# Optimization experiments

Hardware: AMD Instinct MI355X
Metric: run time of the kernel (lower is better)

## Reference

```python
import jax, jax.numpy as jnp
import numpy as np

N, E, F, H, O, G = 50000, 800000, 50, 512, 121, 20
EPS = 1e-5


def _lin(k, out_f, in_f):
    return jax.random.normal(k, (out_f, in_f), jnp.float32) / np.sqrt(in_f)


def setup_inputs() -> dict:
    key = jax.random.key(0)
    ks = jax.random.split(key, 32)
    inp = {
        "x": jax.random.normal(ks[0], (N, F), jnp.float32),
        "edge_index": jax.random.randint(ks[1], (2, E), 0, N, jnp.int64 if jax.config.jax_enable_x64 else jnp.int32),
        "batch": jnp.sort(jax.random.randint(ks[2], (N,), 0, G, jnp.int32)),
    }
    dims = [(F, H), (H, H), (H, H), (H, H), (H, O)]
    ki = 3
    for i, (fi, fo) in enumerate(dims, start=1):
        inp[f"W{i}l"] = _lin(ks[ki], fo, fi); ki += 1
        inp[f"W{i}r"] = _lin(ks[ki], fo, fi); ki += 1
        inp[f"b{i}"] = jnp.zeros((fo,), jnp.float32)
    for i in range(1, 5):
        inp[f"g{i}"] = jnp.ones((H,), jnp.float32)    # GraphNorm weight
        inp[f"bn{i}"] = jnp.zeros((H,), jnp.float32)  # GraphNorm bias
        inp[f"a{i}"] = jnp.ones((H,), jnp.float32)    # GraphNorm mean_scale
    return inp


def _sage(x, src, dst, inv_deg, Wl, Wr, b):
    # mean aggregation of neighbor messages x[src] at dst, then two linears
    agg = jax.ops.segment_sum(x[src], dst, num_segments=N) * inv_deg  # [N, Fin]
    return agg @ Wl.T + x @ Wr.T + b


def _gnorm(x, batch, inv_sz, w, b, alpha):
    mean = jax.ops.segment_sum(x, batch, num_segments=G) * inv_sz  # [G, C]
    out = x - alpha * mean[batch]
    var = jax.ops.segment_sum(out * out, batch, num_segments=G) * inv_sz
    return out * jax.lax.rsqrt(var[batch] + EPS) * w + b


def reference(x, edge_index, batch,
              W1l, W1r, b1, W2l, W2r, b2, W3l, W3r, b3, W4l, W4r, b4, W5l, W5r, b5,
              g1, bn1, a1, g2, bn2, a2, g3, bn3, a3, g4, bn4, a4):
    src, dst = edge_index[0], edge_index[1]
    deg = jax.ops.segment_sum(jnp.ones((E,), jnp.float32), dst, num_segments=N)
    inv_deg = (1.0 / jnp.maximum(deg, 1.0))[:, None]
    sz = jax.ops.segment_sum(jnp.ones((N,), jnp.float32), batch, num_segments=G)
    inv_sz = (1.0 / jnp.maximum(sz, 1.0))[:, None]

    h = _sage(x, src, dst, inv_deg, W1l, W1r, b1)
    h = jax.nn.relu(_gnorm(h, batch, inv_sz, g1, bn1, a1))  # dropout=identity (eval)
    h = _sage(h, src, dst, inv_deg, W2l, W2r, b2)
    h = jax.nn.relu(_gnorm(h, batch, inv_sz, g2, bn2, a2))
    h = _sage(h, src, dst, inv_deg, W3l, W3r, b3)
    h = jax.nn.relu(_gnorm(h, batch, inv_sz, g3, bn3, a3))
    h = _sage(h, src, dst, inv_deg, W4l, W4r, b4)
    h = jax.nn.relu(_gnorm(h, batch, inv_sz, g4, bn4, a4))
    return _sage(h, src, dst, inv_deg, W5l, W5r, b5)
```

## Files before the change

### kernel.cpp

```cpp
#include <hip/hip_runtime.h>
#include <cstddef>
#include <cstdint>

#define N_NODES 50000
#define N_EDGES 800000
#define F_IN 50
#define K1PAD 64
#define H_DIM 512
#define O_DIM 121
#define N_GROUPS 20
#define EPSV 1e-5f
#define M_PAD 50048
#define M_TILES 391

#define STAT_SPLITS 32
#define SCAN_BLK 256
#define SCAN_NBLK ((N_NODES + SCAN_BLK - 1) / SCAN_BLK)
#define WALL_EL 1769472

typedef unsigned short u16;
typedef __attribute__((ext_vector_type(8))) short short8;
typedef __attribute__((ext_vector_type(8))) unsigned short u16x8;
typedef __attribute__((ext_vector_type(4))) float f32x4;

__device__ __forceinline__ float b2f(u16 u) {
  union { unsigned int i; float f; } v; v.i = ((unsigned int)u) << 16; return v.f;
}
__device__ __forceinline__ u16 f2b(float f) {
  union { float f; unsigned int i; } v; v.f = f;
  unsigned int x = v.i;
  return (u16)((x + 0x7fffu + ((x >> 16) & 1u)) >> 16);
}

__device__ __forceinline__ void gl_lds16(const void* g, void* l) {
  __builtin_amdgcn_global_load_lds(
      (__attribute__((address_space(1))) void*)(g),
      (__attribute__((address_space(3))) void*)(l), 16, 0, 0);
}


__global__ void k_deg(const int* __restrict__ dst, int* __restrict__ deg) {
  int e = blockIdx.x * blockDim.x + threadIdx.x;
  if (e < N_EDGES) atomicAdd(&deg[dst[e]], 1);
}

__global__ void k_scan1(const int* __restrict__ deg, int* __restrict__ off,
                        int* __restrict__ bsum) {
  __shared__ int buf[SCAN_BLK];
  int gid = blockIdx.x * SCAN_BLK + threadIdx.x;
  buf[threadIdx.x] = (gid < N_NODES) ? deg[gid] : 0;
  __syncthreads();
  for (int d = 1; d < SCAN_BLK; d <<= 1) {
    int t = (threadIdx.x >= d) ? buf[threadIdx.x - d] : 0;
    __syncthreads();
    buf[threadIdx.x] += t;
    __syncthreads();
  }
  if (gid < N_NODES) off[gid + 1] = buf[threadIdx.x];
  if (threadIdx.x == SCAN_BLK - 1) bsum[blockIdx.x] = buf[threadIdx.x];
}

__global__ void k_scan2(int* __restrict__ bsum) {
  __shared__ int buf[256];
  int t = threadIdx.x;
  buf[t] = (t < SCAN_NBLK) ? bsum[t] : 0;
  __syncthreads();
  for (int d = 1; d < 256; d <<= 1) {
    int v = (t >= d) ? buf[t - d] : 0;
    __syncthreads();
    buf[t] += v;
    __syncthreads();
  }
  if (t < SCAN_NBLK) bsum[t] = buf[t];
}

__global__ void k_scan3prep(int* __restrict__ off, const int* __restrict__ bsum,
                            const int* __restrict__ deg, float* __restrict__ inv_deg,
                            int* __restrict__ cursor) {
  int gid = blockIdx.x * SCAN_BLK + threadIdx.x;
  if (gid < N_NODES) {
    int add = (blockIdx.x > 0) ? bsum[blockIdx.x - 1] : 0;
    int v = off[gid + 1] + add;
    off[gid + 1] = v;
    if (gid + 1 < N_NODES) cursor[gid + 1] = v;
    inv_deg[gid] = 1.0f / (float)max(deg[gid], 1);
  }
  if (gid == 0) { off[0] = 0; cursor[0] = 0; }
}

__global__ void k_scatter(const int* __restrict__ src, const int* __restrict__ dst,
                          int* __restrict__ cursor, int* __restrict__ csr_src) {
  int e = blockIdx.x * blockDim.x + threadIdx.x;
  if (e < N_EDGES) {
    int p = atomicAdd(&cursor[dst[e]], 1);
    csr_src[p] = src[e];
  }
}

__global__ void k_gbounds(const int* __restrict__ batch, int* __restrict__ gstart,
                          float* __restrict__ inv_sz) {
  int g = threadIdx.x;
  if (g <= N_GROUPS) {
    int lo = 0, hi = N_NODES;
    while (lo < hi) {
      int mid = (lo + hi) >> 1;
      if (batch[mid] < g) lo = mid + 1; else hi = mid;
    }
    gstart[g] = lo;
  }
  __syncthreads();
  if (g < N_GROUPS) {
    int sz = gstart[g + 1] - gstart[g];
    inv_sz[g] = 1.0f / (float)max(sz, 1);
  }
}


__global__ void k_xpad(const float* __restrict__ x, u16* __restrict__ xb) {
  int i = blockIdx.x * blockDim.x + threadIdx.x;
  if (i >= M_PAD * K1PAD) return;
  int r = i >> 6, c = i & (K1PAD - 1);
  float v = (r < N_NODES && c < F_IN) ? x[r * F_IN + c] : 0.f;
  xb[i] = f2b(v);
}

struct WcSrc { const float* p[10]; };
__global__ void k_wconv_all(WcSrc s, u16* __restrict__ wall) {
  int idx = blockIdx.x * blockDim.x + threadIdx.x;
  if (idx >= WALL_EL) return;
  const int seg_start[10] = {0, 32768, 65536, 327680, 589824, 851968,
                             1114112, 1376256, 1638400, 1703936};
  const int jr[10]  = {512, 512, 512, 512, 512, 512, 512, 512, 121, 121};
  const int kin[10] = {50, 50, 512, 512, 512, 512, 512, 512, 512, 512};
  const int ksh[10] = {6, 6, 9, 9, 9, 9, 9, 9, 9, 9};
  int sgi = 0;
#pragma unroll
  for (int t = 1; t < 10; ++t)
    if (idx >= seg_start[t]) sgi = t;
  int local = idx - seg_start[sgi];
  int j = local >> ksh[sgi];
  int k = local & ((1 << ksh[sgi]) - 1);
  float v = (j < jr[sgi] && k < kin[sgi]) ? s.p[sgi][j * kin[sgi] + k] : 0.f;
  wall[idx] = f2b(v);
}


__global__ void k_agg_small(const u16* __restrict__ xb, const int* __restrict__ off,
                            const int* __restrict__ srcs, const float* __restrict__ inv_deg,
                            u16* __restrict__ agg) {
  int n = blockIdx.x;
  int f = threadIdx.x;
  int b = off[n], e = off[n + 1];
  float s = 0.f;
  for (int i = b; i < e; ++i) s += b2f(xb[(size_t)srcs[i] * K1PAD + f]);
  agg[(size_t)n * K1PAD + f] = f2b(s * inv_deg[n]);
}

__global__ __launch_bounds__(256) void k_agg512(
    const u16* __restrict__ h, const int* __restrict__ off,
    const int* __restrict__ srcs, const float* __restrict__ inv_deg,
    u16* __restrict__ agg) {
  int n = blockIdx.x * 4 + threadIdx.y;
  if (n >= N_NODES) return;
  int t = threadIdx.x;
  int b = off[n], e = off[n + 1];
  float a[8] = {0.f, 0.f, 0.f, 0.f, 0.f, 0.f, 0.f, 0.f};
  int i = b;
  for (; i + 8 <= e; i += 8) {
    u16x8 v0 = ((const u16x8*)(h + (size_t)srcs[i + 0] * H_DIM))[t];
    u16x8 v1 = ((const u16x8*)(h + (size_t)srcs[i + 1] * H_DIM))[t];
    u16x8 v2 = ((const u16x8*)(h + (size_t)srcs[i + 2] * H_DIM))[t];
    u16x8 v3 = ((const u16x8*)(h + (size_t)srcs[i + 3] * H_DIM))[t];
    u16x8 v4 = ((const u16x8*)(h + (size_t)srcs[i + 4] * H_DIM))[t];
    u16x8 v5 = ((const u16x8*)(h + (size_t)srcs[i + 5] * H_DIM))[t];
    u16x8 v6 = ((const u16x8*)(h + (size_t)srcs[i + 6] * H_DIM))[t];
    u16x8 v7 = ((const u16x8*)(h + (size_t)srcs[i + 7] * H_DIM))[t];
#pragma unroll
    for (int j = 0; j < 8; ++j)
      a[j] += ((b2f(v0[j]) + b2f(v1[j])) + (b2f(v2[j]) + b2f(v3[j]))) +
              ((b2f(v4[j]) + b2f(v5[j])) + (b2f(v6[j]) + b2f(v7[j])));
  }
  for (; i < e; ++i) {
    u16x8 v0 = ((const u16x8*)(h + (size_t)srcs[i] * H_DIM))[t];
#pragma unroll
    for (int j = 0; j < 8; ++j) a[j] += b2f(v0[j]);
  }
  float w = inv_deg[n];
  u16x8 r;
#pragma unroll
  for (int j = 0; j < 8; ++j) r[j] = f2b(a[j] * w);
  ((u16x8*)(agg + (size_t)n * H_DIM))[t] = r;
}

__global__ __launch_bounds__(256) void k_agg_final(
    const u16* __restrict__ Plb, const float* __restrict__ Prf,
    const int* __restrict__ off, const int* __restrict__ srcs,
    const float* __restrict__ inv_deg, const float* __restrict__ bias,
    float* __restrict__ out) {
  int n = blockIdx.x * 8 + (threadIdx.x >> 5);
  if (n >= N_NODES) return;
  int l = threadIdx.x & 31;
  int c0 = l * 4;
  int b = off[n], e = off[n + 1];
  float a0 = 0.f, a1 = 0.f, a2 = 0.f, a3 = 0.f;
  int i = b;
  for (; i + 2 <= e; i += 2) {
    ushort4 v0 = ((const ushort4*)(Plb + (size_t)srcs[i] * 128))[l];
    ushort4 v1 = ((const ushort4*)(Plb + (size_t)srcs[i + 1] * 128))[l];
    a0 += b2f(v0.x) + b2f(v1.x); a1 += b2f(v0.y) + b2f(v1.y);
    a2 += b2f(v0.z) + b2f(v1.z); a3 += b2f(v0.w) + b2f(v1.w);
  }
  if (i < e) {
    ushort4 v0 = ((const ushort4*)(Plb + (size_t)srcs[i] * 128))[l];
    a0 += b2f(v0.x); a1 += b2f(v0.y); a2 += b2f(v0.z); a3 += b2f(v0.w);
  }
  float w = inv_deg[n];
  float4 pr = ((const float4*)(Prf + (size_t)n * 128))[l];
  float r0 = a0 * w + pr.x, r1 = a1 * w + pr.y;
  float r2 = a2 * w + pr.z, r3 = a3 * w + pr.w;
  size_t ob = (size_t)n * O_DIM;
  if (c0 + 0 < O_DIM) out[ob + c0 + 0] = r0 + bias[c0 + 0];
  if (c0 + 1 < O_DIM) out[ob + c0 + 1] = r1 + bias[c0 + 1];
  if (c0 + 2 < O_DIM) out[ob + c0 + 2] = r2 + bias[c0 + 2];
  if (c0 + 3 < O_DIM) out[ob + c0 + 3] = r3 + bias[c0 + 3];
}


#define TM 128
#define TK 32

template <int JB, bool DUAL, int OUTMODE>
__global__ __launch_bounds__(256) void k_gemm_mfma(
    const u16* __restrict__ A, const u16* __restrict__ X,
    const u16* __restrict__ Wl, const u16* __restrict__ Wr,
    const float* __restrict__ bias, void* __restrict__ C0,
    void* __restrict__ C1, int K, int Jreal) {
  __shared__ u16 As[TM * TK];
  __shared__ u16 Ls[TM * TK];
  __shared__ u16 Xs[DUAL ? TM * TK : 1];
  __shared__ u16 Rs[DUAL ? TM * TK : 1];

  int id = blockIdx.x;
  const int nfull = (M_TILES >> 3) * 8 * JB;
  int m_t, j_t;
  if (id < nfull) {
    m_t = (id / (8 * JB)) * 8 + (id & 7);
    j_t = (id >> 3) & (JB - 1);
  } else {
    int rem = id - nfull;
    const int nrem = M_TILES & 7;
    m_t = (M_TILES & ~7) + rem % nrem;
    j_t = rem / nrem;
  }
  int m0 = m_t * TM;
  int j0 = j_t * 128;

  int tid = threadIdx.x;
  int lane = tid & 63;
  int wave = tid >> 6;
  int quad = lane >> 4;
  int lr = lane & 15;
  int wm = (wave & 1) * 64;
  int wn = (wave >> 1) * 64;

  f32x4 acc[4][4] = {};

  int sr = tid >> 2;
  int sc = (tid & 3) * 8;
  size_t moff0 = (size_t)(m0 + sr) * K + sc;
  size_t moff1 = moff0 + (size_t)64 * K;
  size_t joff0 = (size_t)(j0 + sr) * K + sc;
  size_t joff1 = joff0 + (size_t)64 * K;
  const int dofs = tid * 8;

  for (int k0 = 0; k0 < K; k0 += TK) {
    __syncthreads();
    gl_lds16(A + moff0 + k0, As + dofs);
    gl_lds16(A + moff1 + k0, As + 2048 + dofs);
    gl_lds16(Wl + joff0 + k0, Ls + dofs);
    gl_lds16(Wl + joff1 + k0, Ls + 2048 + dofs);
    if constexpr (DUAL) {
      gl_lds16(X + moff0 + k0, Xs + dofs);
      gl_lds16(X + moff1 + k0, Xs + 2048 + dofs);
      gl_lds16(Wr + joff0 + k0, Rs + dofs);
      gl_lds16(Wr + joff1 + k0, Rs + 2048 + dofs);
    }
    __syncthreads();
    short8 af[4], lf[4];
#pragma unroll
    for (int t = 0; t < 4; ++t) {
      af[t] = *(const short8*)(As + (wm + t * 16 + lr) * TK + quad * 8);
      lf[t] = *(const short8*)(Ls + (wn + t * 16 + lr) * TK + quad * 8);
    }
#pragma unroll
    for (int ti = 0; ti < 4; ++ti)
#pragma unroll
      for (int tj = 0; tj < 4; ++tj)
        acc[ti][tj] = __builtin_amdgcn_mfma_f32_16x16x32_bf16(
            af[ti], lf[tj], acc[ti][tj], 0, 0, 0);
    if constexpr (DUAL) {
      short8 xf[4], rf[4];
#pragma unroll
      for (int t = 0; t < 4; ++t) {
        xf[t] = *(const short8*)(Xs + (wm + t * 16 + lr) * TK + quad * 8);
        rf[t] = *(const short8*)(Rs + (wn + t * 16 + lr) * TK + quad * 8);
      }
#pragma unroll
      for (int ti = 0; ti < 4; ++ti)
#pragma unroll
        for (int tj = 0; tj < 4; ++tj)
          acc[ti][tj] = __builtin_amdgcn_mfma_f32_16x16x32_bf16(
              xf[ti], rf[tj], acc[ti][tj], 0, 0, 0);
    }
  }

#pragma unroll
  for (int tj = 0; tj < 4; ++tj) {
    int gcol = j0 + wn + tj * 16 + lr;
    float bv = 0.f;
    if constexpr (OUTMODE == 0) bv = (gcol < Jreal) ? bias[gcol] : 0.f;
#pragma unroll
    for (int ti = 0; ti < 4; ++ti) {
      f32x4 v = acc[ti][tj];
#pragma unroll
      for (int r = 0; r < 4; ++r) {
        int grow = m0 + wm + ti * 16 + quad * 4 + r;
        if constexpr (OUTMODE == 0) {
          if (gcol < Jreal)
            ((u16*)C0)[(size_t)grow * Jreal + gcol] = f2b(v[r] + bv);
        } else {
          if (gcol < 128)
            ((u16*)C0)[(size_t)grow * 128 + gcol] = f2b(v[r]);
          else
            ((float*)C1)[(size_t)grow * 128 + (gcol - 128)] = v[r];
        }
      }
    }
  }
}


__global__ __launch_bounds__(512) void k_stats(
    const u16* __restrict__ h, const int* __restrict__ gstart,
    float* __restrict__ ssum, float* __restrict__ ssq) {
  int g = blockIdx.x;
  int sp = blockIdx.y;
  int f = threadIdx.x;
  int b = gstart[g], e = gstart[g + 1];
  int len = e - b;
  int chunk = (len + STAT_SPLITS - 1) / STAT_SPLITS;
  int lo = b + sp * chunk;
  int hi = min(lo + chunk, e);
  if (lo >= hi) return;
  float s = 0.f, q = 0.f;
  for (int n = lo; n < hi; ++n) {
    float v = b2f(h[(size_t)n * H_DIM + f]);
    s += v; q += v * v;
  }
  atomicAdd(&ssum[g * H_DIM + f], s);
  atomicAdd(&ssq[g * H_DIM + f], q);
}

__global__ void k_apply(u16* __restrict__ h, const int* __restrict__ batch,
                        const float* __restrict__ ssum, const float* __restrict__ ssq,
                        const float* __restrict__ inv_sz, const float* __restrict__ gw,
                        const float* __restrict__ gb, const float* __restrict__ alpha) {
  int tid = blockIdx.x * blockDim.x + threadIdx.x;
  if (tid >= N_NODES * (H_DIM / 8)) return;
  int n = tid >> 6;
  int c0 = (tid & 63) << 3;
  int g = batch[n];
  float is = inv_sz[g];
  u16x8 hv = *(const u16x8*)(h + (size_t)n * H_DIM + c0);
  u16x8 out;
#pragma unroll
  for (int j = 0; j < 8; ++j) {
    int f = c0 + j;
    float m = ssum[g * H_DIM + f] * is;
    float a = alpha[f];
    float ex2 = ssq[g * H_DIM + f] * is;
    float var = fmaxf(ex2 - a * (2.f - a) * m * m, 0.f);
    float o = b2f(hv[j]) - a * m;
    float y = o * rsqrtf(var + EPSV) * gw[f] + gb[f];
    out[j] = f2b(fmaxf(y, 0.f));
  }
  *(u16x8*)(h + (size_t)n * H_DIM + c0) = out;
}


extern "C" void kernel_launch(void* const* d_in, const int* in_sizes, int n_in,
                              void* d_out, int out_size, void* d_ws, size_t ws_size,
                              hipStream_t stream) {
  const float* x = (const float*)d_in[0];
  const int* edge = (const int*)d_in[1];
  const int* batch = (const int*)d_in[2];
  const float *Wl[5], *Wr[5], *bb[5];
  for (int i = 0; i < 5; ++i) {
    Wl[i] = (const float*)d_in[3 + 3 * i];
    Wr[i] = (const float*)d_in[4 + 3 * i];
    bb[i] = (const float*)d_in[5 + 3 * i];
  }
  const float *gamma[4], *beta[4], *alpha[4];
  for (int i = 0; i < 4; ++i) {
    gamma[i] = (const float*)d_in[18 + 3 * i];
    beta[i]  = (const float*)d_in[19 + 3 * i];
    alpha[i] = (const float*)d_in[20 + 3 * i];
  }
  const int* srcv = edge;
  const int* dstv = edge + N_EDGES;

  char* base = (char*)d_ws;
  size_t off = 0;
  auto carve = [&](size_t bytes) -> char* {
    char* p = base + off;
    off = (off + bytes + 255) & ~(size_t)255;
    return p;
  };
  int* deg       = (int*)carve((size_t)N_NODES * 4);
  float* inv_deg = (float*)carve((size_t)N_NODES * 4);
  int* csr_off   = (int*)carve((size_t)(N_NODES + 1) * 4);
  int* cursor    = (int*)carve((size_t)N_NODES * 4);
  int* csr_src   = (int*)carve((size_t)N_EDGES * 4);
  int* bsum      = (int*)carve((size_t)SCAN_NBLK * 4);
  int* gstart    = (int*)carve((size_t)(N_GROUPS + 1) * 4);
  float* inv_sz  = (float*)carve((size_t)N_GROUPS * 4);
  float* stats   = (float*)carve((size_t)4 * 2 * N_GROUPS * H_DIM * 4);
  u16* xb        = (u16*)carve((size_t)M_PAD * K1PAD * 2);
  u16* aggx      = (u16*)carve((size_t)M_PAD * K1PAD * 2);
  u16* h0        = (u16*)carve((size_t)M_PAD * H_DIM * 2);
  u16* h1        = (u16*)carve((size_t)M_PAD * H_DIM * 2);
  u16* h2        = (u16*)carve((size_t)M_PAD * H_DIM * 2);
  u16* wall      = (u16*)carve((size_t)WALL_EL * 2);
  (void)ws_size; (void)in_sizes; (void)n_in; (void)out_size;

  u16* w1lb = wall;
  u16* w1rb = wall + 32768;
  u16* w2lb = wall + 65536;
  u16* w2rb = wall + 327680;
  u16* w3lb = wall + 589824;
  u16* w3rb = wall + 851968;
  u16* w4lb = wall + 1114112;
  u16* w4rb = wall + 1376256;
  u16* w5cat = wall + 1638400;

  u16* Plb = h1;
  float* Prf = (float*)((char*)h1 + (size_t)M_PAD * 128 * 2);

  hipMemsetAsync(deg, 0, (size_t)N_NODES * 4, stream);
  k_deg<<<(N_EDGES + 255) / 256, 256, 0, stream>>>(dstv, deg);
  k_scan1<<<SCAN_NBLK, SCAN_BLK, 0, stream>>>(deg, csr_off, bsum);
  k_scan2<<<1, 256, 0, stream>>>(bsum);
  k_scan3prep<<<SCAN_NBLK, SCAN_BLK, 0, stream>>>(csr_off, bsum, deg, inv_deg, cursor);
  k_scatter<<<(N_EDGES + 255) / 256, 256, 0, stream>>>(srcv, dstv, cursor, csr_src);
  k_gbounds<<<1, 64, 0, stream>>>(batch, gstart, inv_sz);
  k_xpad<<<(M_PAD * K1PAD + 255) / 256, 256, 0, stream>>>(x, xb);

  WcSrc ws_src;
  ws_src.p[0] = Wl[0]; ws_src.p[1] = Wr[0];
  ws_src.p[2] = Wl[1]; ws_src.p[3] = Wr[1];
  ws_src.p[4] = Wl[2]; ws_src.p[5] = Wr[2];
  ws_src.p[6] = Wl[3]; ws_src.p[7] = Wr[3];
  ws_src.p[8] = Wl[4]; ws_src.p[9] = Wr[4];
  k_wconv_all<<<(WALL_EL + 255) / 256, 256, 0, stream>>>(ws_src, wall);

  hipMemsetAsync(stats, 0, (size_t)4 * 2 * N_GROUPS * H_DIM * 4, stream);

  const int nblk_main = M_TILES * 4;
  const int nblk_l5   = M_TILES * 2;
  dim3 aggblk(64, 4);
  int aggrid = (N_NODES + 3) / 4;

  auto norm = [&](u16* h, int l) {
    float* ss = stats + (size_t)l * 2 * N_GROUPS * H_DIM;
    float* sq = ss + N_GROUPS * H_DIM;
    k_stats<<<dim3(N_GROUPS, STAT_SPLITS), 512, 0, stream>>>(h, gstart, ss, sq);
    k_apply<<<(N_NODES * (H_DIM / 8) + 255) / 256, 256, 0, stream>>>(
        h, batch, ss, sq, inv_sz, gamma[l], beta[l], alpha[l]);
  };

  k_agg_small<<<N_NODES, 64, 0, stream>>>(xb, csr_off, csr_src, inv_deg, aggx);
  k_gemm_mfma<4, true, 0><<<nblk_main, 256, 0, stream>>>(
      aggx, xb, w1lb, w1rb, bb[0], h0, nullptr, K1PAD, H_DIM);
  norm(h0, 0);

  k_agg512<<<aggrid, aggblk, 0, stream>>>(h0, csr_off, csr_src, inv_deg, h1);
  k_gemm_mfma<4, true, 0><<<nblk_main, 256, 0, stream>>>(
      h1, h0, w2lb, w2rb, bb[1], h2, nullptr, H_DIM, H_DIM);
  norm(h2, 1);

  k_agg512<<<aggrid, aggblk, 0, stream>>>(h2, csr_off, csr_src, inv_deg, h0);
  k_gemm_mfma<4, true, 0><<<nblk_main, 256, 0, stream>>>(
      h0, h2, w3lb, w3rb, bb[2], h1, nullptr, H_DIM, H_DIM);
  norm(h1, 2);

  k_agg512<<<aggrid, aggblk, 0, stream>>>(h1, csr_off, csr_src, inv_deg, h2);
  k_gemm_mfma<4, true, 0><<<nblk_main, 256, 0, stream>>>(
      h2, h1, w4lb, w4rb, bb[3], h0, nullptr, H_DIM, H_DIM);
  norm(h0, 3);

  k_gemm_mfma<2, false, 1><<<nblk_l5, 256, 0, stream>>>(
      h0, nullptr, w5cat, nullptr, nullptr, Plb, Prf, H_DIM, 256);
  k_agg_final<<<(N_NODES + 7) / 8, 256, 0, stream>>>(
      Plb, Prf, csr_off, csr_src, inv_deg, bb[4], (float*)d_out);
}
```

Before: 1.200 ms.

## Fuse GraphNorm stats into GEMM epilogue, split edge aggregation, merge setup kernels

The GEMM epilogue now accumulates per-group sums and squared sums with wave shuffles and atomics, which removes the separate stats pass over h. A small precompute kernel turns those into per-group scale and shift tables for a simpler apply pass. The 512-wide aggregation now splits each node's edge list across two half-blocks and combines them through shared memory. The setup kernels are also merged: scan2 with gbounds, and xpad with the weight conversion. The costs are atomic contention in the epilogue, statistics computed from fp32 values before bf16 rounding, and an extra barrier in aggregation.

```diff
diff --git a/kernel.cpp b/kernel.cpp
--- a/kernel.cpp
+++ b/kernel.cpp
@@ -13,10 +13,10 @@
 #define M_PAD 50048
 #define M_TILES 391
 
-#define STAT_SPLITS 32
 #define SCAN_BLK 256
 #define SCAN_NBLK ((N_NODES + SCAN_BLK - 1) / SCAN_BLK)
 #define WALL_EL 1769472
+#define XB_EL (M_PAD * K1PAD)
 
 typedef unsigned short u16;
 typedef __attribute__((ext_vector_type(8))) short short8;
@@ -60,18 +60,35 @@
   if (threadIdx.x == SCAN_BLK - 1) bsum[blockIdx.x] = buf[threadIdx.x];
 }
 
-__global__ void k_scan2(int* __restrict__ bsum) {
-  __shared__ int buf[256];
+__global__ void k_scan2_gbounds(int* __restrict__ bsum, const int* __restrict__ batch,
+                                int* __restrict__ gstart, float* __restrict__ inv_sz) {
   int t = threadIdx.x;
-  buf[t] = (t < SCAN_NBLK) ? bsum[t] : 0;
-  __syncthreads();
-  for (int d = 1; d < 256; d <<= 1) {
-    int v = (t >= d) ? buf[t - d] : 0;
+  if (blockIdx.x == 0) {
+    __shared__ int buf[256];
+    buf[t] = (t < SCAN_NBLK) ? bsum[t] : 0;
     __syncthreads();
-    buf[t] += v;
+    for (int d = 1; d < 256; d <<= 1) {
+      int v = (t >= d) ? buf[t - d] : 0;
+      __syncthreads();
+      buf[t] += v;
+      __syncthreads();
+    }
+    if (t < SCAN_NBLK) bsum[t] = buf[t];
+  } else {
+    if (t <= N_GROUPS) {
+      int lo = 0, hi = N_NODES;
+      while (lo < hi) {
+        int mid = (lo + hi) >> 1;
+        if (batch[mid] < t) lo = mid + 1; else hi = mid;
+      }
+      gstart[t] = lo;
+    }
     __syncthreads();
-  }
-  if (t < SCAN_NBLK) bsum[t] = buf[t];
+    if (t < N_GROUPS) {
+      int sz = gstart[t + 1] - gstart[t];
+      inv_sz[t] = 1.0f / (float)max(sz, 1);
+    }
+  }
 }
 
 __global__ void k_scan3prep(int* __restrict__ off, const int* __restrict__ bsum,
@@ -97,36 +114,17 @@
   }
 }
 
-__global__ void k_gbounds(const int* __restrict__ batch, int* __restrict__ gstart,
-                          float* __restrict__ inv_sz) {
-  int g = threadIdx.x;
-  if (g <= N_GROUPS) {
-    int lo = 0, hi = N_NODES;
-    while (lo < hi) {
-      int mid = (lo + hi) >> 1;
-      if (batch[mid] < g) lo = mid + 1; else hi = mid;
-    }
-    gstart[g] = lo;
-  }
-  __syncthreads();
-  if (g < N_GROUPS) {
-    int sz = gstart[g + 1] - gstart[g];
-    inv_sz[g] = 1.0f / (float)max(sz, 1);
-  }
-}
-
-
-__global__ void k_xpad(const float* __restrict__ x, u16* __restrict__ xb) {
-  int i = blockIdx.x * blockDim.x + threadIdx.x;
-  if (i >= M_PAD * K1PAD) return;
-  int r = i >> 6, c = i & (K1PAD - 1);
-  float v = (r < N_NODES && c < F_IN) ? x[r * F_IN + c] : 0.f;
-  xb[i] = f2b(v);
-}
-
 struct WcSrc { const float* p[10]; };
-__global__ void k_wconv_all(WcSrc s, u16* __restrict__ wall) {
+__global__ void k_convert_all(const float* __restrict__ x, WcSrc s,
+                              u16* __restrict__ xb, u16* __restrict__ wall) {
   int idx = blockIdx.x * blockDim.x + threadIdx.x;
+  if (idx < XB_EL) {
+    int r = idx >> 6, c = idx & (K1PAD - 1);
+    float v = (r < N_NODES && c < F_IN) ? x[r * F_IN + c] : 0.f;
+    xb[idx] = f2b(v);
+    return;
+  }
+  idx -= XB_EL;
   if (idx >= WALL_EL) return;
   const int seg_start[10] = {0, 32768, 65536, 327680, 589824, 851968,
                              1114112, 1376256, 1638400, 1703936};
@@ -156,40 +154,49 @@
   agg[(size_t)n * K1PAD + f] = f2b(s * inv_deg[n]);
 }
 
-__global__ __launch_bounds__(256) void k_agg512(
+__global__ __launch_bounds__(512) void k_agg512(
     const u16* __restrict__ h, const int* __restrict__ off,
     const int* __restrict__ srcs, const float* __restrict__ inv_deg,
     u16* __restrict__ agg) {
-  int n = blockIdx.x * 4 + threadIdx.y;
-  if (n >= N_NODES) return;
+  __shared__ float part[4][64][8];
+  int slot = threadIdx.y >> 1;
+  int sub = threadIdx.y & 1;
+  int n = blockIdx.x * 4 + slot;
   int t = threadIdx.x;
-  int b = off[n], e = off[n + 1];
   float a[8] = {0.f, 0.f, 0.f, 0.f, 0.f, 0.f, 0.f, 0.f};
-  int i = b;
-  for (; i + 8 <= e; i += 8) {
-    u16x8 v0 = ((const u16x8*)(h + (size_t)srcs[i + 0] * H_DIM))[t];
-    u16x8 v1 = ((const u16x8*)(h + (size_t)srcs[i + 1] * H_DIM))[t];
-    u16x8 v2 = ((const u16x8*)(h + (size_t)srcs[i + 2] * H_DIM))[t];
-    u16x8 v3 = ((const u16x8*)(h + (size_t)srcs[i + 3] * H_DIM))[t];
-    u16x8 v4 = ((const u16x8*)(h + (size_t)srcs[i + 4] * H_DIM))[t];
-    u16x8 v5 = ((const u16x8*)(h + (size_t)srcs[i + 5] * H_DIM))[t];
-    u16x8 v6 = ((const u16x8*)(h + (size_t)srcs[i + 6] * H_DIM))[t];
-    u16x8 v7 = ((const u16x8*)(h + (size_t)srcs[i + 7] * H_DIM))[t];
-#pragma unroll
-    for (int j = 0; j < 8; ++j)
-      a[j] += ((b2f(v0[j]) + b2f(v1[j])) + (b2f(v2[j]) + b2f(v3[j]))) +
-              ((b2f(v4[j]) + b2f(v5[j])) + (b2f(v6[j]) + b2f(v7[j])));
-  }
-  for (; i < e; ++i) {
-    u16x8 v0 = ((const u16x8*)(h + (size_t)srcs[i] * H_DIM))[t];
-#pragma unroll
-    for (int j = 0; j < 8; ++j) a[j] += b2f(v0[j]);
-  }
-  float w = inv_deg[n];
-  u16x8 r;
-#pragma unroll
-  for (int j = 0; j < 8; ++j) r[j] = f2b(a[j] * w);
-  ((u16x8*)(agg + (size_t)n * H_DIM))[t] = r;
+  if (n < N_NODES) {
+    int b = off[n], e = off[n + 1];
+    int half = (e - b + 1) >> 1;
+    int lo = b + sub * half;
+    int hi = min(lo + half, e);
+    int i = lo;
+    for (; i + 4 <= hi; i += 4) {
+      u16x8 v0 = ((const u16x8*)(h + (size_t)srcs[i + 0] * H_DIM))[t];
+      u16x8 v1 = ((const u16x8*)(h + (size_t)srcs[i + 1] * H_DIM))[t];
+      u16x8 v2 = ((const u16x8*)(h + (size_t)srcs[i + 2] * H_DIM))[t];
+      u16x8 v3 = ((const u16x8*)(h + (size_t)srcs[i + 3] * H_DIM))[t];
+#pragma unroll
+      for (int j = 0; j < 8; ++j)
+        a[j] += (b2f(v0[j]) + b2f(v1[j])) + (b2f(v2[j]) + b2f(v3[j]));
+    }
+    for (; i < hi; ++i) {
+      u16x8 v0 = ((const u16x8*)(h + (size_t)srcs[i] * H_DIM))[t];
+#pragma unroll
+      for (int j = 0; j < 8; ++j) a[j] += b2f(v0[j]);
+    }
+  }
+  if (sub == 1) {
+#pragma unroll
+    for (int j = 0; j < 8; ++j) part[slot][t][j] = a[j];
+  }
+  __syncthreads();
+  if (sub == 0 && n < N_NODES) {
+    float w = inv_deg[n];
+    u16x8 r;
+#pragma unroll
+    for (int j = 0; j < 8; ++j) r[j] = f2b((a[j] + part[slot][t][j]) * w);
+    ((u16x8*)(agg + (size_t)n * H_DIM))[t] = r;
+  }
 }
 
 __global__ __launch_bounds__(256) void k_agg_final(
@@ -234,7 +241,8 @@
     const u16* __restrict__ A, const u16* __restrict__ X,
     const u16* __restrict__ Wl, const u16* __restrict__ Wr,
     const float* __restrict__ bias, void* __restrict__ C0,
-    void* __restrict__ C1, int K, int Jreal) {
+    void* __restrict__ C1, const int* __restrict__ batch,
+    float* __restrict__ ssum, float* __restrict__ ssq, int K) {
   __shared__ u16 As[TM * TK];
   __shared__ u16 Ls[TM * TK];
   __shared__ u16 Xs[DUAL ? TM * TK : 1];
@@ -314,21 +322,72 @@
     }
   }
 
-#pragma unroll
-  for (int tj = 0; tj < 4; ++tj) {
-    int gcol = j0 + wn + tj * 16 + lr;
-    float bv = 0.f;
-    if constexpr (OUTMODE == 0) bv = (gcol < Jreal) ? bias[gcol] : 0.f;
-#pragma unroll
-    for (int ti = 0; ti < 4; ++ti) {
-      f32x4 v = acc[ti][tj];
-#pragma unroll
-      for (int r = 0; r < 4; ++r) {
-        int grow = m0 + wm + ti * 16 + quad * 4 + r;
-        if constexpr (OUTMODE == 0) {
-          if (gcol < Jreal)
-            ((u16*)C0)[(size_t)grow * Jreal + gcol] = f2b(v[r] + bv);
+  if constexpr (OUTMODE == 0) {
+    int glo = batch[m0];
+    int lastrow = m0 + TM - 1;
+    bool fast = (lastrow < N_NODES) && (batch[lastrow] == glo);
+#pragma unroll
+    for (int tj = 0; tj < 4; ++tj) {
+      int gcol = j0 + wn + tj * 16 + lr;
+      float bv = bias[gcol];
+      float s = 0.f, q = 0.f;
+#pragma unroll
+      for (int ti = 0; ti < 4; ++ti) {
+        f32x4 v = acc[ti][tj];
+        int rbase = m0 + wm + ti * 16 + quad * 4;
+        if (fast) {
+#pragma unroll
+          for (int r = 0; r < 4; ++r) {
+            float val = v[r] + bv;
+            ((u16*)C0)[(size_t)(rbase + r) * H_DIM + gcol] = f2b(val);
+            s += val; q += val * val;
+          }
         } else {
+          if (rbase + 3 < N_NODES && batch[rbase] == batch[rbase + 3]) {
+            float s4 = 0.f, q4 = 0.f;
+#pragma unroll
+            for (int r = 0; r < 4; ++r) {
+              float val = v[r] + bv;
+              ((u16*)C0)[(size_t)(rbase + r) * H_DIM + gcol] = f2b(val);
+              s4 += val; q4 += val * val;
+            }
+            int g = batch[rbase];
+            atomicAdd(&ssum[g * H_DIM + gcol], s4);
+            atomicAdd(&ssq[g * H_DIM + gcol], q4);
+          } else {
+#pragma unroll
+            for (int r = 0; r < 4; ++r) {
+              int grow = rbase + r;
+              if (grow < N_NODES) {
+                float val = v[r] + bv;
+                ((u16*)C0)[(size_t)grow * H_DIM + gcol] = f2b(val);
+                int g = batch[grow];
+                atomicAdd(&ssum[g * H_DIM + gcol], val);
+                atomicAdd(&ssq[g * H_DIM + gcol], val * val);
+              }
+            }
+          }
+        }
+      }
+      if (fast) {
+        s += __shfl_xor(s, 16); s += __shfl_xor(s, 32);
+        q += __shfl_xor(q, 16); q += __shfl_xor(q, 32);
+        if (quad == 0) {
+          atomicAdd(&ssum[glo * H_DIM + gcol], s);
+          atomicAdd(&ssq[glo * H_DIM + gcol], q);
+        }
+      }
+    }
+  } else {
+#pragma unroll
+    for (int tj = 0; tj < 4; ++tj) {
+      int gcol = j0 + wn + tj * 16 + lr;
+#pragma unroll
+      for (int ti = 0; ti < 4; ++ti) {
+        f32x4 v = acc[ti][tj];
+#pragma unroll
+        for (int r = 0; r < 4; ++r) {
+          int grow = m0 + wm + ti * 16 + quad * 4 + r;
           if (gcol < 128)
             ((u16*)C0)[(size_t)grow * 128 + gcol] = f2b(v[r]);
           else
@@ -340,48 +399,37 @@
 }
 
 
-__global__ __launch_bounds__(512) void k_stats(
-    const u16* __restrict__ h, const int* __restrict__ gstart,
-    float* __restrict__ ssum, float* __restrict__ ssq) {
-  int g = blockIdx.x;
-  int sp = blockIdx.y;
-  int f = threadIdx.x;
-  int b = gstart[g], e = gstart[g + 1];
-  int len = e - b;
-  int chunk = (len + STAT_SPLITS - 1) / STAT_SPLITS;
-  int lo = b + sp * chunk;
-  int hi = min(lo + chunk, e);
-  if (lo >= hi) return;
-  float s = 0.f, q = 0.f;
-  for (int n = lo; n < hi; ++n) {
-    float v = b2f(h[(size_t)n * H_DIM + f]);
-    s += v; q += v * v;
-  }
-  atomicAdd(&ssum[g * H_DIM + f], s);
-  atomicAdd(&ssq[g * H_DIM + f], q);
+__global__ void k_precomp(const float* __restrict__ ssum, const float* __restrict__ ssq,
+                          const float* __restrict__ inv_sz, const float* __restrict__ gw,
+                          const float* __restrict__ gb, const float* __restrict__ alpha,
+                          float* __restrict__ S, float* __restrict__ T) {
+  int idx = blockIdx.x * blockDim.x + threadIdx.x;
+  if (idx >= N_GROUPS * H_DIM) return;
+  int g = idx >> 9;
+  int c = idx & (H_DIM - 1);
+  float is = inv_sz[g];
+  float m = ssum[idx] * is;
+  float a = alpha[c];
+  float var = fmaxf(ssq[idx] * is - a * (2.f - a) * m * m, 0.f);
+  float inv = rsqrtf(var + EPSV);
+  float sc = inv * gw[c];
+  S[idx] = sc;
+  T[idx] = gb[c] - a * m * sc;
 }
 
 __global__ void k_apply(u16* __restrict__ h, const int* __restrict__ batch,
-                        const float* __restrict__ ssum, const float* __restrict__ ssq,
-                        const float* __restrict__ inv_sz, const float* __restrict__ gw,
-                        const float* __restrict__ gb, const float* __restrict__ alpha) {
+                        const float* __restrict__ S, const float* __restrict__ T) {
   int tid = blockIdx.x * blockDim.x + threadIdx.x;
   if (tid >= N_NODES * (H_DIM / 8)) return;
   int n = tid >> 6;
   int c0 = (tid & 63) << 3;
   int g = batch[n];
-  float is = inv_sz[g];
   u16x8 hv = *(const u16x8*)(h + (size_t)n * H_DIM + c0);
   u16x8 out;
 #pragma unroll
   for (int j = 0; j < 8; ++j) {
     int f = c0 + j;
-    float m = ssum[g * H_DIM + f] * is;
-    float a = alpha[f];
-    float ex2 = ssq[g * H_DIM + f] * is;
-    float var = fmaxf(ex2 - a * (2.f - a) * m * m, 0.f);
-    float o = b2f(hv[j]) - a * m;
-    float y = o * rsqrtf(var + EPSV) * gw[f] + gb[f];
+    float y = b2f(hv[j]) * S[g * H_DIM + f] + T[g * H_DIM + f];
     out[j] = f2b(fmaxf(y, 0.f));
   }
   *(u16x8*)(h + (size_t)n * H_DIM + c0) = out;
@@ -425,8 +473,10 @@
   int* gstart    = (int*)carve((size_t)(N_GROUPS + 1) * 4);
   float* inv_sz  = (float*)carve((size_t)N_GROUPS * 4);
   float* stats   = (float*)carve((size_t)4 * 2 * N_GROUPS * H_DIM * 4);
-  u16* xb        = (u16*)carve((size_t)M_PAD * K1PAD * 2);
-  u16* aggx      = (u16*)carve((size_t)M_PAD * K1PAD * 2);
+  float* Sbuf    = (float*)carve((size_t)N_GROUPS * H_DIM * 4);
+  float* Tbuf    = (float*)carve((size_t)N_GROUPS * H_DIM * 4);
+  u16* xb        = (u16*)carve((size_t)XB_EL * 2);
+  u16* aggx      = (u16*)carve((size_t)XB_EL * 2);
   u16* h0        = (u16*)carve((size_t)M_PAD * H_DIM * 2);
   u16* h1        = (u16*)carve((size_t)M_PAD * H_DIM * 2);
   u16* h2        = (u16*)carve((size_t)M_PAD * H_DIM * 2);
@@ -449,11 +499,9 @@
   hipMemsetAsync(deg, 0, (size_t)N_NODES * 4, stream);
   k_deg<<<(N_EDGES + 255) / 256, 256, 0, stream>>>(dstv, deg);
   k_scan1<<<SCAN_NBLK, SCAN_BLK, 0, stream>>>(deg, csr_off, bsum);
-  k_scan2<<<1, 256, 0, stream>>>(bsum);
+  k_scan2_gbounds<<<2, 256, 0, stream>>>(bsum, batch, gstart, inv_sz);
   k_scan3prep<<<SCAN_NBLK, SCAN_BLK, 0, stream>>>(csr_off, bsum, deg, inv_deg, cursor);
   k_scatter<<<(N_EDGES + 255) / 256, 256, 0, stream>>>(srcv, dstv, cursor, csr_src);
-  k_gbounds<<<1, 64, 0, stream>>>(batch, gstart, inv_sz);
-  k_xpad<<<(M_PAD * K1PAD + 255) / 256, 256, 0, stream>>>(x, xb);
 
   WcSrc ws_src;
   ws_src.p[0] = Wl[0]; ws_src.p[1] = Wr[0];
@@ -461,45 +509,51 @@
   ws_src.p[4] = Wl[2]; ws_src.p[5] = Wr[2];
   ws_src.p[6] = Wl[3]; ws_src.p[7] = Wr[3];
   ws_src.p[8] = Wl[4]; ws_src.p[9] = Wr[4];
-  k_wconv_all<<<(WALL_EL + 255) / 256, 256, 0, stream>>>(ws_src, wall);
+  k_convert_all<<<(XB_EL + WALL_EL + 255) / 256, 256, 0, stream>>>(x, ws_src, xb, wall);
 
   hipMemsetAsync(stats, 0, (size_t)4 * 2 * N_GROUPS * H_DIM * 4, stream);
 
   const int nblk_main = M_TILES * 4;
   const int nblk_l5   = M_TILES * 2;
-  dim3 aggblk(64, 4);
+  dim3 aggblk(64, 8);
   int aggrid = (N_NODES + 3) / 4;
 
   auto norm = [&](u16* h, int l) {
     float* ss = stats + (size_t)l * 2 * N_GROUPS * H_DIM;
     float* sq = ss + N_GROUPS * H_DIM;
-    k_stats<<<dim3(N_GROUPS, STAT_SPLITS), 512, 0, stream>>>(h, gstart, ss, sq);
+    k_precomp<<<(N_GROUPS * H_DIM + 255) / 256, 256, 0, stream>>>(
+        ss, sq, inv_sz, gamma[l], beta[l], alpha[l], Sbuf, Tbuf);
     k_apply<<<(N_NODES * (H_DIM / 8) + 255) / 256, 256, 0, stream>>>(
-        h, batch, ss, sq, inv_sz, gamma[l], beta[l], alpha[l]);
+        h, batch, Sbuf, Tbuf);
   };
+  auto stat_ptr = [&](int l) { return stats + (size_t)l * 2 * N_GROUPS * H_DIM; };
 
   k_agg_small<<<N_NODES, 64, 0, stream>>>(xb, csr_off, csr_src, inv_deg, aggx);
   k_gemm_mfma<4, true, 0><<<nblk_main, 256, 0, stream>>>(
-      aggx, xb, w1lb, w1rb, bb[0], h0, nullptr, K1PAD, H_DIM);
+      aggx, xb, w1lb, w1rb, bb[0], h0, nullptr, batch,
+      stat_ptr(0), stat_ptr(0) + N_GROUPS * H_DIM, K1PAD);
   norm(h0, 0);
 
   k_agg512<<<aggrid, aggblk, 0, stream>>>(h0, csr_off, csr_src, inv_deg, h1);
   k_gemm_mfma<4, true, 0><<<nblk_main, 256, 0, stream>>>(
-      h1, h0, w2lb, w2rb, bb[1], h2, nullptr, H_DIM, H_DIM);
+      h1, h0, w2lb, w2rb, bb[1], h2, nullptr, batch,
+      stat_ptr(1), stat_ptr(1) + N_GROUPS * H_DIM, H_DIM);
   norm(h2, 1);
 
   k_agg512<<<aggrid, aggblk, 0, stream>>>(h2, csr_off, csr_src, inv_deg, h0);
   k_gemm_mfma<4, true, 0><<<nblk_main, 256, 0, stream>>>(
-      h0, h2, w3lb, w3rb, bb[2], h1, nullptr, H_DIM, H_DIM);
+      h0, h2, w3lb, w3rb, bb[2], h1, nullptr, batch,
+      stat_ptr(2), stat_ptr(2) + N_GROUPS * H_DIM, H_DIM);
   norm(h1, 2);
 
   k_agg512<<<aggrid, aggblk, 0, stream>>>(h1, csr_off, csr_src, inv_deg, h2);
   k_gemm_mfma<4, true, 0><<<nblk_main, 256, 0, stream>>>(
-      h2, h1, w4lb, w4rb, bb[3], h0, nullptr, H_DIM, H_DIM);
+      h2, h1, w4lb, w4rb, bb[3], h0, nullptr, batch,
+      stat_ptr(3), stat_ptr(3) + N_GROUPS * H_DIM, H_DIM);
   norm(h0, 3);
 
   k_gemm_mfma<2, false, 1><<<nblk_l5, 256, 0, stream>>>(
-      h0, nullptr, w5cat, nullptr, nullptr, Plb, Prf, H_DIM, 256);
+      h0, nullptr, w5cat, nullptr, nullptr, Plb, Prf, nullptr, nullptr, nullptr, H_DIM);
   k_agg_final<<<(N_NODES + 7) / 8, 256, 0, stream>>>(
       Plb, Prf, csr_off, csr_src, inv_deg, bb[4], (float*)d_out);
 }
```

Result: faster. 1.088 ms (-9.3%).
